# Kernel tuning notes

Hardware: AMD Instinct MI355X
Metric: run time of the kernel (lower is better)

## Reference

```python
import jax, jax.numpy as jnp
import numpy as np

N_NODES = 100000
T = 1024        # number of visits / hyperedges (GRU sequence length)
IN = 128        # in_channel
HID = 256       # hid_channel


def setup_inputs() -> dict:
    key = jax.random.key(0)
    ks = jax.random.split(key, 7)
    X = jax.random.normal(ks[0], (N_NODES, IN), dtype=jnp.float32)
    H = jax.random.uniform(ks[1], (N_NODES, T), dtype=jnp.float32)
    s = 1.0 / np.sqrt(HID)  # torch default GRU init scale
    w_ih = jax.random.uniform(ks[2], (3 * HID, IN), jnp.float32, -s, s)
    w_hh = jax.random.uniform(ks[3], (3 * HID, HID), jnp.float32, -s, s)
    b_ih = jax.random.uniform(ks[4], (3 * HID,), jnp.float32, -s, s)
    b_hh = jax.random.uniform(ks[5], (3 * HID,), jnp.float32, -s, s)
    w_attn = jax.random.uniform(ks[6], (HID,), jnp.float32, -s, s)
    return {"X": X, "H": H, "w_ih": w_ih, "w_hh": w_hh,
            "b_ih": b_ih, "b_hh": b_hh, "w_attn": w_attn}


def _gru(visit_emb, w_ih, w_hh, b_ih, b_hh):
    # Precompute input-side gates for all timesteps: [T, 3H]
    gx = visit_emb @ w_ih.T + b_ih

    def step(h, gx_t):
        gh = h @ w_hh.T + b_hh
        xr, xz, xn = jnp.split(gx_t, 3)
        hr, hz, hn = jnp.split(gh, 3)
        r = jax.nn.sigmoid(xr + hr)
        z = jax.nn.sigmoid(xz + hz)
        n = jnp.tanh(xn + r * hn)
        h_new = (1.0 - z) * n + z * h
        return h_new, h_new

    h0 = jnp.zeros((HID,), visit_emb.dtype)
    _, hs = jax.lax.scan(step, h0, gx)
    return hs  # [T, HID]


def reference(X, H, w_ih, w_hh, b_ih, b_hh, w_attn):
    # visit_emb = H.T @ X : [T, IN]
    visit_emb = H.T @ X
    hs = _gru(visit_emb, w_ih, w_hh, b_ih, b_hh)          # [T, HID]
    alpha = jax.nn.softmax(hs @ w_attn)                    # [T]
    # sum(diag(alpha) @ hs, 0) == alpha-weighted sum of hidden states
    return alpha @ hs                                      # [HID]
```

## Files before the change

### kernel.cpp

```cpp
#include <hip/hip_runtime.h>
#include <hip/hip_fp16.h>

typedef _Float16 half8 __attribute__((ext_vector_type(8)));
typedef _Float16 half2v __attribute__((ext_vector_type(2)));
typedef float f32x4 __attribute__((ext_vector_type(4)));

#define T_STEPS 1024
#define INC 128
#define HIDC 256
#define G3 768
#define NN 100000
#define KSPLIT 32
#define NCHUNK 3125
#define XS_STRIDE 144

__device__ __forceinline__ float dpp_xor1(float v){
  int t = __builtin_amdgcn_update_dpp(0, __float_as_int(v), 0xB1, 0xF, 0xF, true);
  return __int_as_float(t);
}

__global__ __launch_bounds__(512) void k_phase1(const float* __restrict__ X,
                                                const float* __restrict__ Hm,
                                                float* __restrict__ part){
  const int bid = blockIdx.x;
  const int xcd = bid & 7;
  const int idx = bid >> 3;
  const int ks  = xcd * 4 + (idx & 3);
  const int tt  = idx >> 2;
  const int t0 = tt * 128;
  const int nbeg = ks * NCHUNK;
  const int nend = nbeg + NCHUNK;
  __shared__ float Hs[16][128];
  __shared__ float Xs[16 * XS_STRIDE];
  const int tid = threadIdx.x;
  const int tx = tid & 15;
  const int ty = tid >> 4;
  const int sr = tid >> 5;
  const int sc = tid & 31;
  const int xskew = tx * 8 + (tx >> 2) * 4;

  float acc[4][8];
  #pragma unroll
  for (int r = 0; r < 4; r++)
    #pragma unroll
    for (int q = 0; q < 8; q++) acc[r][q] = 0.f;

  float4 hv = make_float4(0.f,0.f,0.f,0.f), xv = make_float4(0.f,0.f,0.f,0.f);
  {
    int n = nbeg + sr;
    if (n < nend){
      hv = *(const float4*)(Hm + (size_t)n * T_STEPS + t0 + sc * 4);
      xv = *(const float4*)(X  + (size_t)n * INC + sc * 4);
    }
  }

  for (int n0 = nbeg; n0 < nend; n0 += 16){
    __builtin_amdgcn_s_barrier();
    asm volatile("" ::: "memory");
    *(float4*)&Hs[sr][sc * 4] = hv;
    {
      int g = sc >> 1, hf = sc & 1;
      *(float4*)&Xs[sr * XS_STRIDE + g * 8 + (g >> 2) * 4 + hf * 4] = xv;
    }
    asm volatile("s_waitcnt lgkmcnt(0)" ::: "memory");
    __builtin_amdgcn_s_barrier();
    asm volatile("" ::: "memory");

    {
      int nn = n0 + 16 + sr;
      hv = make_float4(0.f,0.f,0.f,0.f);
      xv = make_float4(0.f,0.f,0.f,0.f);
      if (nn < nend){
        hv = *(const float4*)(Hm + (size_t)nn * T_STEPS + t0 + sc * 4);
        xv = *(const float4*)(X  + (size_t)nn * INC + sc * 4);
      }
    }

    #pragma unroll
    for (int i = 0; i < 16; i++){
      float4 h4 = *(const float4*)&Hs[i][ty * 4];
      float4 x0 = *(const float4*)&Xs[i * XS_STRIDE + xskew];
      float4 x1 = *(const float4*)&Xs[i * XS_STRIDE + xskew + 4];
      float xr[8] = {x0.x,x0.y,x0.z,x0.w,x1.x,x1.y,x1.z,x1.w};
      float hr[4] = {h4.x,h4.y,h4.z,h4.w};
      #pragma unroll
      for (int r = 0; r < 4; r++)
        #pragma unroll
        for (int q = 0; q < 8; q++)
          acc[r][q] += hr[r] * xr[q];
    }
  }
  #pragma unroll
  for (int r = 0; r < 4; r++){
    size_t o = ((size_t)ks * T_STEPS + t0 + ty * 4 + r) * INC + tx * 8;
    *(float4*)&part[o]     = make_float4(acc[r][0], acc[r][1], acc[r][2], acc[r][3]);
    *(float4*)&part[o + 4] = make_float4(acc[r][4], acc[r][5], acc[r][6], acc[r][7]);
  }
}

__global__ __launch_bounds__(256) void k_reduce(const float* __restrict__ part,
                                                float* __restrict__ ve){
  int idx = blockIdx.x * 256 + threadIdx.x;
  float s = 0.f;
  #pragma unroll
  for (int ks = 0; ks < KSPLIT; ks++) s += part[(size_t)ks * (T_STEPS * INC) + idx];
  ve[idx] = s;
}

__global__ __launch_bounds__(768) void k_gx(const float* __restrict__ ve,
                                            const float* __restrict__ w_ih,
                                            const float* __restrict__ b_ih,
                                            const float* __restrict__ b_hh,
                                            float* __restrict__ gxq){
  const int t = blockIdx.x;
  const int j = threadIdx.x;
  __shared__ float4 v4[32];
  if (j < 32) v4[j] = *(const float4*)(ve + (size_t)t * INC + j * 4);
  __syncthreads();
  const float4* wr = (const float4*)(w_ih + (size_t)j * INC);
  float a0 = 0.f, a1 = 0.f, a2 = 0.f, a3 = 0.f;
  #pragma unroll
  for (int q = 0; q < 32; q++){
    float4 w = wr[q]; float4 v = v4[q];
    a0 += w.x * v.x; a1 += w.y * v.y; a2 += w.z * v.z; a3 += w.w * v.w;
  }
  float bias = b_ih[j] + (j < 512 ? b_hh[j] : 0.f);
  gxq[(size_t)t * 1024 + (j & 255) * 4 + (j >> 8)] = (a0 + a1) + (a2 + a3) + bias;
}

__global__ __attribute__((amdgpu_flat_work_group_size(512, 512),
                          amdgpu_waves_per_eu(2, 2)))
void k_gru(const float* __restrict__ w_hh,
           const float* __restrict__ b_hh,
           const float* __restrict__ gxq,
           float* __restrict__ hs){
  const int tid  = threadIdx.x;
  const int unit = tid >> 1;
  const int ks   = tid & 1;
  const int k0   = ks * 128;

  __shared__ _Float16 hbuf[2][256];

  half2v Bp[3][64];
  #pragma unroll
  for (int g = 0; g < 3; g++){
    const float* wr = w_hh + (size_t)(g * 256 + unit) * HIDC + k0;
    #pragma unroll
    for (int c = 0; c < 32; c++){
      float4 v = *(const float4*)(wr + c * 4);
      half2v p0; p0[0] = (_Float16)v.x; p0[1] = (_Float16)v.y;
      half2v p1; p1[0] = (_Float16)v.z; p1[1] = (_Float16)v.w;
      Bp[g][2 * c]     = p0;
      Bp[g][2 * c + 1] = p1;
      if (c & 1) __builtin_amdgcn_sched_barrier(0);
    }
  }
  const float bn = b_hh[512 + unit];
  float hprev = 0.f;
  if (tid < 256) hbuf[0][tid] = (_Float16)0.f;
  __syncthreads();

  f32x4 gq = *(const f32x4*)(gxq + (size_t)unit * 4);

  for (int t = 0; t < T_STEPS; t++){
    const _Float16* hb = &hbuf[t & 1][k0];
    float ar0 = 0.f, ar1 = 0.f, az0 = 0.f, az1 = 0.f, an0 = 0.f, an1 = 0.f;
    #pragma unroll
    for (int c = 0; c < 16; c++){
      half8 hv = *(const half8*)(hb + c * 8);
      #pragma unroll
      for (int q = 0; q < 4; q++){
        half2v hp; hp[0] = hv[2 * q]; hp[1] = hv[2 * q + 1];
        if (c & 1){
          ar1 = __builtin_amdgcn_fdot2(hp, Bp[0][4 * c + q], ar1, false);
          az1 = __builtin_amdgcn_fdot2(hp, Bp[1][4 * c + q], az1, false);
          an1 = __builtin_amdgcn_fdot2(hp, Bp[2][4 * c + q], an1, false);
        } else {
          ar0 = __builtin_amdgcn_fdot2(hp, Bp[0][4 * c + q], ar0, false);
          az0 = __builtin_amdgcn_fdot2(hp, Bp[1][4 * c + q], az0, false);
          an0 = __builtin_amdgcn_fdot2(hp, Bp[2][4 * c + q], an0, false);
        }
      }
    }
    f32x4 gq_n = *(const f32x4*)(gxq + (size_t)(t + 1) * 1024 + unit * 4);

    float dr = ar0 + ar1; dr += dpp_xor1(dr);
    float dz = az0 + az1; dz += dpp_xor1(dz);
    float dn = an0 + an1; dn += dpp_xor1(dn);

    float r = 1.f / (1.f + __expf(-(gq[0] + dr)));
    float z = 1.f / (1.f + __expf(-(gq[1] + dz)));
    float pre = gq[2] + r * (dn + bn);
    float ax = fabsf(pre);
    float e = __expf(-2.f * ax);
    float th = (1.f - e) / (1.f + e);
    float n = copysignf(th, pre);
    float hnew = n + z * (hprev - n);
    hprev = hnew;
    if (ks == 0){
      hbuf[(t + 1) & 1][unit] = (_Float16)hnew;
      hs[(size_t)t * HIDC + unit] = hnew;
    }
    gq = gq_n;
    __syncthreads();
  }
}

__global__ __launch_bounds__(64) void k_logits(const float* __restrict__ hs,
                                               const float* __restrict__ w_attn,
                                               float* __restrict__ logits){
  int t = blockIdx.x;
  int l = threadIdx.x;
  float4 hv = *(const float4*)(hs + (size_t)t * HIDC + l * 4);
  float4 wv = *(const float4*)(w_attn + l * 4);
  float p = hv.x * wv.x + hv.y * wv.y + hv.z * wv.z + hv.w * wv.w;
  #pragma unroll
  for (int o = 32; o > 0; o >>= 1) p += __shfl_down(p, o);
  if (l == 0) logits[t] = p;
}

__global__ __launch_bounds__(1024) void k_attn(const float* __restrict__ logits,
                                               const float* __restrict__ hs,
                                               float* __restrict__ out){
  __shared__ float sm[1024];
  __shared__ float al[1024];
  __shared__ float ps[4][HIDC];
  int tid = threadIdx.x;
  float lg = logits[tid];
  sm[tid] = lg; __syncthreads();
  for (int s = 512; s > 0; s >>= 1){
    if (tid < s) sm[tid] = fmaxf(sm[tid], sm[tid + s]);
    __syncthreads();
  }
  float mx = sm[0]; __syncthreads();
  float e = __expf(lg - mx);
  sm[tid] = e; __syncthreads();
  for (int s = 512; s > 0; s >>= 1){
    if (tid < s) sm[tid] += sm[tid + s];
    __syncthreads();
  }
  float inv = 1.f / sm[0];
  al[tid] = e * inv;
  __syncthreads();
  int c = tid & 255; int tq = tid >> 8;
  float acc = 0.f;
  for (int t = tq; t < T_STEPS; t += 4) acc += al[t] * hs[(size_t)t * HIDC + c];
  ps[tq][c] = acc; __syncthreads();
  if (tid < HIDC) out[tid] = (ps[0][tid] + ps[1][tid]) + (ps[2][tid] + ps[3][tid]);
}

extern "C" void kernel_launch(void* const* d_in, const int* in_sizes, int n_in,
                              void* d_out, int out_size, void* d_ws, size_t ws_size,
                              hipStream_t stream){
  const float* X      = (const float*)d_in[0];
  const float* Hm     = (const float*)d_in[1];
  const float* w_ih   = (const float*)d_in[2];
  const float* w_hh   = (const float*)d_in[3];
  const float* b_ih   = (const float*)d_in[4];
  const float* b_hh   = (const float*)d_in[5];
  const float* w_attn = (const float*)d_in[6];
  float* out = (float*)d_out;

  float* ws     = (float*)d_ws;
  float* part   = ws;
  float* ve     = part + 4194304;
  float* gxq    = ve + 131072;
  float* hs     = gxq + 1049600;
  float* logits = hs + 262144;

  k_phase1<<<256, 512, 0, stream>>>(X, Hm, part);
  k_reduce<<<512, 256, 0, stream>>>(part, ve);
  k_gx<<<1024, 768, 0, stream>>>(ve, w_ih, b_ih, b_hh, gxq);
  k_gru<<<1, 512, 0, stream>>>(w_hh, b_hh, gxq, hs);
  k_logits<<<1024, 64, 0, stream>>>(hs, w_attn, logits);
  k_attn<<<1, 1024, 0, stream>>>(logits, hs, out);
}
```

Measured before the change: 2.211 ms.

## Broadcast GRU hidden state via readlane and split phase1 into finer T tiles

The GRU kernel now assigns each wave a group of 64 units and half of the K range. Each lane loads one packed half2 of the hidden state, and readlane broadcasts it to the rest of the wave, replacing per-thread LDS vector reads. The two K halves are combined through an LDS partial buffer with two barriers per step, replacing the DPP xor reduction, and only the ks==0 waves compute the gates. Separately, phase1 tiles T in chunks of 64 instead of 128 and launches 512 blocks for more parallelism, which lowers per-thread register reuse and leaves half the lanes idle during the H loads.

```diff
diff --git a/kernel.cpp b/kernel.cpp
--- a/kernel.cpp
+++ b/kernel.cpp
@@ -14,11 +14,6 @@
 #define NCHUNK 3125
 #define XS_STRIDE 144
 
-__device__ __forceinline__ float dpp_xor1(float v){
-  int t = __builtin_amdgcn_update_dpp(0, __float_as_int(v), 0xB1, 0xF, 0xF, true);
-  return __int_as_float(t);
-}
-
 __global__ __launch_bounds__(512) void k_phase1(const float* __restrict__ X,
                                                 const float* __restrict__ Hm,
                                                 float* __restrict__ part){
@@ -27,10 +22,10 @@
   const int idx = bid >> 3;
   const int ks  = xcd * 4 + (idx & 3);
   const int tt  = idx >> 2;
-  const int t0 = tt * 128;
+  const int t0  = tt * 64;
   const int nbeg = ks * NCHUNK;
   const int nend = nbeg + NCHUNK;
-  __shared__ float Hs[16][128];
+  __shared__ float Hs[16][64];
   __shared__ float Xs[16 * XS_STRIDE];
   const int tid = threadIdx.x;
   const int tx = tid & 15;
@@ -39,9 +34,9 @@
   const int sc = tid & 31;
   const int xskew = tx * 8 + (tx >> 2) * 4;
 
-  float acc[4][8];
-  #pragma unroll
-  for (int r = 0; r < 4; r++)
+  float acc[2][8];
+  #pragma unroll
+  for (int r = 0; r < 2; r++)
     #pragma unroll
     for (int q = 0; q < 8; q++) acc[r][q] = 0.f;
 
@@ -49,7 +44,7 @@
   {
     int n = nbeg + sr;
     if (n < nend){
-      hv = *(const float4*)(Hm + (size_t)n * T_STEPS + t0 + sc * 4);
+      if (sc < 16) hv = *(const float4*)(Hm + (size_t)n * T_STEPS + t0 + sc * 4);
       xv = *(const float4*)(X  + (size_t)n * INC + sc * 4);
     }
   }
@@ -57,7 +52,7 @@
   for (int n0 = nbeg; n0 < nend; n0 += 16){
     __builtin_amdgcn_s_barrier();
     asm volatile("" ::: "memory");
-    *(float4*)&Hs[sr][sc * 4] = hv;
+    if (sc < 16) *(float4*)&Hs[sr][sc * 4] = hv;
     {
       int g = sc >> 1, hf = sc & 1;
       *(float4*)&Xs[sr * XS_STRIDE + g * 8 + (g >> 2) * 4 + hf * 4] = xv;
@@ -71,28 +66,27 @@
       hv = make_float4(0.f,0.f,0.f,0.f);
       xv = make_float4(0.f,0.f,0.f,0.f);
       if (nn < nend){
-        hv = *(const float4*)(Hm + (size_t)nn * T_STEPS + t0 + sc * 4);
+        if (sc < 16) hv = *(const float4*)(Hm + (size_t)nn * T_STEPS + t0 + sc * 4);
         xv = *(const float4*)(X  + (size_t)nn * INC + sc * 4);
       }
     }
 
     #pragma unroll
     for (int i = 0; i < 16; i++){
-      float4 h4 = *(const float4*)&Hs[i][ty * 4];
+      float2 h2 = *(const float2*)&Hs[i][ty * 2];
       float4 x0 = *(const float4*)&Xs[i * XS_STRIDE + xskew];
       float4 x1 = *(const float4*)&Xs[i * XS_STRIDE + xskew + 4];
       float xr[8] = {x0.x,x0.y,x0.z,x0.w,x1.x,x1.y,x1.z,x1.w};
-      float hr[4] = {h4.x,h4.y,h4.z,h4.w};
       #pragma unroll
-      for (int r = 0; r < 4; r++)
-        #pragma unroll
-        for (int q = 0; q < 8; q++)
-          acc[r][q] += hr[r] * xr[q];
-    }
-  }
-  #pragma unroll
-  for (int r = 0; r < 4; r++){
-    size_t o = ((size_t)ks * T_STEPS + t0 + ty * 4 + r) * INC + tx * 8;
+      for (int q = 0; q < 8; q++){
+        acc[0][q] += h2.x * xr[q];
+        acc[1][q] += h2.y * xr[q];
+      }
+    }
+  }
+  #pragma unroll
+  for (int r = 0; r < 2; r++){
+    size_t o = ((size_t)ks * T_STEPS + t0 + ty * 2 + r) * INC + tx * 8;
     *(float4*)&part[o]     = make_float4(acc[r][0], acc[r][1], acc[r][2], acc[r][3]);
     *(float4*)&part[o + 4] = make_float4(acc[r][4], acc[r][5], acc[r][6], acc[r][7]);
   }
@@ -135,11 +129,15 @@
            const float* __restrict__ gxq,
            float* __restrict__ hs){
   const int tid  = threadIdx.x;
-  const int unit = tid >> 1;
-  const int ks   = tid & 1;
+  const int w    = tid >> 6;
+  const int l    = tid & 63;
+  const int ks   = w >> 2;
+  const int ug   = w & 3;
+  const int unit = ug * 64 + l;
   const int k0   = ks * 128;
 
   __shared__ _Float16 hbuf[2][256];
+  __shared__ float pbuf[4][64][4];
 
   half2v Bp[3][64];
   #pragma unroll
@@ -163,46 +161,52 @@
   f32x4 gq = *(const f32x4*)(gxq + (size_t)unit * 4);
 
   for (int t = 0; t < T_STEPS; t++){
-    const _Float16* hb = &hbuf[t & 1][k0];
+    const int* hb32 = (const int*)&hbuf[t & 1][0];
+    int vh2 = hb32[ks * 64 + l];
+
     float ar0 = 0.f, ar1 = 0.f, az0 = 0.f, az1 = 0.f, an0 = 0.f, an1 = 0.f;
     #pragma unroll
-    for (int c = 0; c < 16; c++){
-      half8 hv = *(const half8*)(hb + c * 8);
-      #pragma unroll
-      for (int q = 0; q < 4; q++){
-        half2v hp; hp[0] = hv[2 * q]; hp[1] = hv[2 * q + 1];
-        if (c & 1){
-          ar1 = __builtin_amdgcn_fdot2(hp, Bp[0][4 * c + q], ar1, false);
-          az1 = __builtin_amdgcn_fdot2(hp, Bp[1][4 * c + q], az1, false);
-          an1 = __builtin_amdgcn_fdot2(hp, Bp[2][4 * c + q], an1, false);
-        } else {
-          ar0 = __builtin_amdgcn_fdot2(hp, Bp[0][4 * c + q], ar0, false);
-          az0 = __builtin_amdgcn_fdot2(hp, Bp[1][4 * c + q], az0, false);
-          an0 = __builtin_amdgcn_fdot2(hp, Bp[2][4 * c + q], an0, false);
-        }
+    for (int j = 0; j < 64; j++){
+      half2v h2 = __builtin_bit_cast(half2v, __builtin_amdgcn_readlane(vh2, j));
+      if (j & 1){
+        ar1 = __builtin_amdgcn_fdot2(h2, Bp[0][j], ar1, false);
+        az1 = __builtin_amdgcn_fdot2(h2, Bp[1][j], az1, false);
+        an1 = __builtin_amdgcn_fdot2(h2, Bp[2][j], an1, false);
+      } else {
+        ar0 = __builtin_amdgcn_fdot2(h2, Bp[0][j], ar0, false);
+        az0 = __builtin_amdgcn_fdot2(h2, Bp[1][j], az0, false);
+        an0 = __builtin_amdgcn_fdot2(h2, Bp[2][j], an0, false);
       }
     }
     f32x4 gq_n = *(const f32x4*)(gxq + (size_t)(t + 1) * 1024 + unit * 4);
 
-    float dr = ar0 + ar1; dr += dpp_xor1(dr);
-    float dz = az0 + az1; dz += dpp_xor1(dz);
-    float dn = an0 + an1; dn += dpp_xor1(dn);
-
-    float r = 1.f / (1.f + __expf(-(gq[0] + dr)));
-    float z = 1.f / (1.f + __expf(-(gq[1] + dz)));
-    float pre = gq[2] + r * (dn + bn);
-    float ax = fabsf(pre);
-    float e = __expf(-2.f * ax);
-    float th = (1.f - e) / (1.f + e);
-    float n = copysignf(th, pre);
-    float hnew = n + z * (hprev - n);
-    hprev = hnew;
+    float dr = ar0 + ar1, dz = az0 + az1, dn = an0 + an1;
+    if (ks == 1){
+      *(float4*)&pbuf[ug][l][0] = make_float4(dr, dz, dn, 0.f);
+    }
+    asm volatile("s_waitcnt lgkmcnt(0)" ::: "memory");
+    __builtin_amdgcn_s_barrier();
+    asm volatile("" ::: "memory");
+
     if (ks == 0){
+      f32x4 p = *(const f32x4*)&pbuf[ug][l][0];
+      dr += p[0]; dz += p[1]; dn += p[2];
+      float r = 1.f / (1.f + __expf(-(gq[0] + dr)));
+      float z = 1.f / (1.f + __expf(-(gq[1] + dz)));
+      float pre = gq[2] + r * (dn + bn);
+      float ax = fabsf(pre);
+      float e = __expf(-2.f * ax);
+      float th = (1.f - e) / (1.f + e);
+      float n = copysignf(th, pre);
+      float hnew = n + z * (hprev - n);
+      hprev = hnew;
       hbuf[(t + 1) & 1][unit] = (_Float16)hnew;
       hs[(size_t)t * HIDC + unit] = hnew;
     }
+    asm volatile("s_waitcnt lgkmcnt(0)" ::: "memory");
+    __builtin_amdgcn_s_barrier();
+    asm volatile("" ::: "memory");
     gq = gq_n;
-    __syncthreads();
   }
 }
 
@@ -268,7 +272,7 @@
   float* hs     = gxq + 1049600;
   float* logits = hs + 262144;
 
-  k_phase1<<<256, 512, 0, stream>>>(X, Hm, part);
+  k_phase1<<<512, 512, 0, stream>>>(X, Hm, part);
   k_reduce<<<512, 256, 0, stream>>>(part, ve);
   k_gx<<<1024, 768, 0, stream>>>(ve, w_ih, b_ih, b_hh, gxq);
   k_gru<<<1, 512, 0, stream>>>(w_hh, b_hh, gxq, hs);
```

Result: slower. 2.650 ms (+19.8%).
